# Optimization experiments

Hardware: AMD Instinct MI355X
Metric: run time of the kernel (lower is better)

The kernel has to match this reference:

```python
import jax, jax.numpy as jnp
import numpy as np

B, N, F_IN, F_OUT = 64, 1024, 200, 200
NEG_SLOPE = 0.2  # PyG GATConv default


def setup_inputs() -> dict:
    key = jax.random.key(0)
    k1, k2, k3, k4, k5 = jax.random.split(key, 5)
    return {
        "x": jax.random.normal(k1, (B, 1, N, F_IN), dtype=jnp.float32),
        "W": jax.random.normal(k2, (F_IN, F_OUT), dtype=jnp.float32) * 0.05,
        "att_src": jax.random.normal(k3, (F_OUT,), dtype=jnp.float32) * 0.05,
        "att_dst": jax.random.normal(k4, (F_OUT,), dtype=jnp.float32) * 0.05,
        "bias": jax.random.normal(k5, (F_OUT,), dtype=jnp.float32) * 0.05,
    }


def reference(x, W, att_src, att_dst, bias):
    # x: [B, 1, N, F_IN]; module flattens to (B*N) nodes but the edge_index
    # only spans node ids 0..N-1 (complete graph minus self loops). PyG's
    # GATConv re-adds self loops for ALL B*N nodes, so:
    #   nodes 0..N-1 : dense softmax attention over all N nodes (incl. self)
    #   nodes >= N   : only the self loop -> out = h_i + bias
    b, _, n, f = x.shape
    xf = x.reshape(b * n, f)
    h = xf @ W                                # [B*N, F_OUT] linear transform

    h0 = h[:n]                                # first graph's nodes
    a_s = h0 @ att_src                        # [N] per-source score
    a_d = h0 @ att_dst                        # [N] per-target score
    # score[i, j] = leaky_relu(a_dst[i] + a_src[j]), softmax over sources j
    scores = jax.nn.leaky_relu(a_d[:, None] + a_s[None, :], negative_slope=NEG_SLOPE)
    alpha = jax.nn.softmax(scores, axis=1)    # [N, N]
    out0 = alpha @ h0 + bias                  # [N, F_OUT]

    out_rest = h[n:] + bias                   # self-loop only -> alpha == 1
    out = jnp.concatenate([out0, out_rest], axis=0)
    return out.reshape(b, n, -1)[:, None]     # [B, 1, N, F_OUT]
```

## Files before the change

kernel.cpp:

```cpp
#include <hip/hip_runtime.h>

#define BATCH 64
#define NNODE 1024
#define FDIM  200
#define MROWS (BATCH * NNODE)
#define NEG_SLOPE 0.2f

#define NKT 7
#define NNT 13
#define FRAGW_BYTES (NKT * NNT * 1024)

typedef short s16x8 __attribute__((ext_vector_type(8)));
typedef float f32x4 __attribute__((ext_vector_type(4)));


__device__ __forceinline__ unsigned int f2bf(float f) {
    unsigned int u = __float_as_uint(f);
    return (u + 0x7fffu + ((u >> 16) & 1u)) >> 16;
}
__device__ __forceinline__ unsigned int pack2(float a, float b) {
    return f2bf(a) | (f2bf(b) << 16);
}
__device__ __forceinline__ float lrelu(float s) {
    return (s > 0.f) ? s : NEG_SLOPE * s;
}

__global__ __launch_bounds__(64) void k_prep(const float* __restrict__ W,
                                             const float* __restrict__ att_src,
                                             const float* __restrict__ att_dst,
                                             unsigned short* __restrict__ fragW,
                                             float* __restrict__ wsv,
                                             float* __restrict__ wdv)
{
    const int b    = blockIdx.x;
    const int lane = threadIdx.x;

    if (b < 91) {
        const int kt   = b / NNT;
        const int nt   = b - kt * NNT;
        const int n    = nt * 16 + (lane & 15);
        const int kb   = kt * 32 + (lane >> 4) * 8;
        s16x8 v;
        #pragma unroll
        for (int j = 0; j < 8; ++j) {
            int k = kb + j;
            float f = (k < FDIM && n < FDIM) ? W[k * FDIM + n] : 0.f;
            v[j] = (short)f2bf(f);
        }
        ((s16x8*)(fragW + (size_t)b * 512))[lane] = v;
    } else {
        const int kk = b - 91;
        const float* Wr = W + kk * FDIM;
        float ps = 0.f, pd = 0.f;
        #pragma unroll
        for (int i = 0; i < 4; ++i) {
            int n = lane + i * 64;
            if (n < FDIM) {
                float wv = Wr[n];
                ps = fmaf(wv, att_src[n], ps);
                pd = fmaf(wv, att_dst[n], pd);
            }
        }
        #pragma unroll
        for (int off = 32; off; off >>= 1) {
            ps += __shfl_down(ps, off);
            pd += __shfl_down(pd, off);
        }
        if (lane == 0) { wsv[kk] = ps; wdv[kk] = pd; }
    }
}

__global__ __launch_bounds__(512, 2) void k_gemm(const float* __restrict__ x,
                                                 const unsigned short* __restrict__ fragW,
                                                 const float* __restrict__ bias,
                                                 const float* __restrict__ wsv,
                                                 const float* __restrict__ wdv,
                                                 float* __restrict__ out,
                                                 unsigned short* __restrict__ h0frag,
                                                 float* __restrict__ a_s,
                                                 float* __restrict__ a_d)
{
    __shared__ __align__(16) unsigned short Bf[FRAGW_BYTES / 2];
    __shared__ float scr[8][16 * 17];
    const int tid  = threadIdx.x;
    const int lane = tid & 63;
    const int w    = __builtin_amdgcn_readfirstlane(tid >> 6);
    const int ln   = lane & 15;
    const int quad = lane >> 4;
    const int R0   = blockIdx.x * 128;
    const int row0 = R0 + w * 16;

    {
        const char* gsrc = (const char*)fragW;
        char* ldst = (char*)&Bf[0];
        #pragma unroll
        for (int r = 0; r < 12; ++r) {
            int off = tid * 16 + r * 8192;
            if (off < FRAGW_BYTES)
                __builtin_amdgcn_global_load_lds(
                    (const __attribute__((address_space(1))) void*)(gsrc + off),
                    (__attribute__((address_space(3))) void*)(ldst + off),
                    16, 0, 0);
        }
    }

    const float* xrow = x + (size_t)(row0 + ln) * FDIM;
    float4 ar[NKT][2];
    #pragma unroll
    for (int kt = 0; kt < NKT; ++kt) {
        if (kt < 6) {
            const float4* ap = (const float4*)(xrow + kt * 32 + quad * 8);
            ar[kt][0] = ap[0]; ar[kt][1] = ap[1];
        } else {
            if (quad == 0) {
                const float4* ap = (const float4*)(xrow + kt * 32);
                ar[kt][0] = ap[0]; ar[kt][1] = ap[1];
            } else {
                ar[kt][0] = make_float4(0.f, 0.f, 0.f, 0.f);
                ar[kt][1] = make_float4(0.f, 0.f, 0.f, 0.f);
            }
        }
    }

    f32x4 acc[NNT];
    #pragma unroll
    for (int nt = 0; nt < NNT; ++nt) acc[nt] = (f32x4){0.f, 0.f, 0.f, 0.f};

    __syncthreads();

    #pragma unroll
    for (int kt = 0; kt < NKT; ++kt) {
        float4 f0 = ar[kt][0], f1 = ar[kt][1];
        unsigned int au[4] = {pack2(f0.x, f0.y), pack2(f0.z, f0.w),
                              pack2(f1.x, f1.y), pack2(f1.z, f1.w)};
        s16x8 a = *(s16x8*)au;
        const unsigned short* bbase = &Bf[kt * NNT * 512];
        #pragma unroll
        for (int nt = 0; nt < NNT; ++nt) {
            s16x8 b = *(const s16x8*)(bbase + nt * 512 + lane * 8);
            acc[nt] = __builtin_amdgcn_mfma_f32_16x16x32_bf16(a, b, acc[nt], 0, 0, 0);
        }
    }

    if (R0 >= NNODE) {
        #pragma unroll
        for (int nt = 0; nt < NNT; ++nt) {
            int col = nt * 16 + ln;
            if (nt < 12 || ln < 8) {
                float bv = bias[col];
                #pragma unroll
                for (int r = 0; r < 4; ++r)
                    out[(size_t)(row0 + quad * 4 + r) * FDIM + col] = acc[nt][r] + bv;
            }
        }
    } else {
        {
            float ps = 0.f, pd = 0.f;
            #pragma unroll
            for (int kt = 0; kt < NKT; ++kt) {
                if (kt < 6 || quad == 0) {
                    float4 f0 = ar[kt][0], f1 = ar[kt][1];
                    const float4* sp = (const float4*)(wsv + kt * 32 + quad * 8);
                    const float4* dp = (const float4*)(wdv + kt * 32 + quad * 8);
                    float4 s0 = sp[0], s1 = sp[1], d0 = dp[0], d1 = dp[1];
                    ps += f0.x*s0.x + f0.y*s0.y + f0.z*s0.z + f0.w*s0.w
                        + f1.x*s1.x + f1.y*s1.y + f1.z*s1.z + f1.w*s1.w;
                    pd += f0.x*d0.x + f0.y*d0.y + f0.z*d0.z + f0.w*d0.w
                        + f1.x*d1.x + f1.y*d1.y + f1.z*d1.z + f1.w*d1.w;
                }
            }
            ps += __shfl_down(ps, 32); ps += __shfl_down(ps, 16);
            pd += __shfl_down(pd, 32); pd += __shfl_down(pd, 16);
            if (lane < 16) {
                a_s[row0 + lane] = ps;
                a_d[row0 + lane] = pd;
            }
        }
        float* scrw = &scr[w][0];
        const int kt2 = row0 >> 5;
        const int lo  = (row0 >> 4) & 1;
        for (int nt = 0; nt < NNT; ++nt) {
            #pragma unroll
            for (int r = 0; r < 4; ++r) scrw[(quad * 4 + r) * 17 + ln] = acc[nt][r];
            __syncthreads();
            if (lane < 32) {
                int oct = lane >> 4, nl = lane & 15;
                uint4 dv;
                dv.x = pack2(scrw[(oct * 8 + 0) * 17 + nl], scrw[(oct * 8 + 1) * 17 + nl]);
                dv.y = pack2(scrw[(oct * 8 + 2) * 17 + nl], scrw[(oct * 8 + 3) * 17 + nl]);
                dv.z = pack2(scrw[(oct * 8 + 4) * 17 + nl], scrw[(oct * 8 + 5) * 17 + nl]);
                dv.w = pack2(scrw[(oct * 8 + 6) * 17 + nl], scrw[(oct * 8 + 7) * 17 + nl]);
                *(uint4*)(h0frag + ((size_t)(kt2 * NNT + nt) * 64 + lo * 32 + lane) * 8) = dv;
            }
            __syncthreads();
        }
    }
}

__global__ __launch_bounds__(256) void k_attn(const unsigned short* __restrict__ h0frag,
                                              const float* __restrict__ a_s,
                                              const float* __restrict__ a_d,
                                              const float* __restrict__ bias,
                                              float* __restrict__ out)
{
    __shared__ __align__(16) float as_s[1024];
    __shared__ float mls[16];
    __shared__ float rls[16];
    __shared__ f32x4 red[3][64];
    const int tid  = threadIdx.x;
    const int lane = tid & 63;
    const int w    = __builtin_amdgcn_readfirstlane(tid >> 6);
    const int ln   = lane & 15;
    const int quad = lane >> 4;
    const int it   = blockIdx.x / NNT;
    const int nt   = blockIdx.x - it * NNT;
    const int i0   = it * 16;

    #pragma unroll
    for (int i = 0; i < 4; ++i) as_s[tid + i * 256] = a_s[tid + i * 256];
    __syncthreads();

    float mx = -1e30f;
    #pragma unroll
    for (int i = 0; i < 16; ++i) mx = fmaxf(mx, as_s[lane + i * 64]);
    #pragma unroll
    for (int off = 32; off; off >>= 1) mx = fmaxf(mx, __shfl_down(mx, off));
    mx = __shfl(mx, 0);

    #pragma unroll
    for (int rr = 0; rr < 4; ++rr) {
        const int r  = w * 4 + rr;
        const float adr = a_d[i0 + r];
        const float mi  = lrelu(adr + mx);
        float sum = 0.f;
        #pragma unroll
        for (int i = 0; i < 16; ++i)
            sum += __expf(lrelu(adr + as_s[lane + i * 64]) - mi);
        #pragma unroll
        for (int off = 32; off; off >>= 1) sum += __shfl_down(sum, off);
        if (lane == 0) { mls[r] = mi; rls[r] = 1.0f / sum; }
    }
    __syncthreads();

    const float ad = a_d[i0 + ln];
    const float mi = mls[ln];

    f32x4 accA = (f32x4){0.f, 0.f, 0.f, 0.f};
    f32x4 accB = (f32x4){0.f, 0.f, 0.f, 0.f};

    #pragma unroll
    for (int k8 = 0; k8 < 8; ++k8) {
        const int kt2 = w * 8 + k8;
        const float4* ap = (const float4*)(as_s + kt2 * 32 + quad * 8);
        float4 f0 = ap[0], f1 = ap[1];
        float e[8] = {f0.x, f0.y, f0.z, f0.w, f1.x, f1.y, f1.z, f1.w};
        #pragma unroll
        for (int j = 0; j < 8; ++j)
            e[j] = __expf(lrelu(ad + e[j]) - mi);
        unsigned int au[4] = {pack2(e[0], e[1]), pack2(e[2], e[3]),
                              pack2(e[4], e[5]), pack2(e[6], e[7])};
        s16x8 afrag = *(s16x8*)au;
        s16x8 b = *(const s16x8*)(h0frag + ((size_t)(kt2 * NNT + nt) * 64 + lane) * 8);
        if (k8 & 1) accB = __builtin_amdgcn_mfma_f32_16x16x32_bf16(afrag, b, accB, 0, 0, 0);
        else        accA = __builtin_amdgcn_mfma_f32_16x16x32_bf16(afrag, b, accA, 0, 0, 0);
    }

    f32x4 acc = accA + accB;
    if (w > 0) red[w - 1][lane] = acc;
    __syncthreads();

    if (w == 0) {
        #pragma unroll
        for (int ww = 0; ww < 3; ++ww) acc += red[ww][lane];
        const int col = nt * 16 + ln;
        if (nt < 12 || ln < 8) {
            float bv = bias[col];
            #pragma unroll
            for (int r = 0; r < 4; ++r) {
                float rl = rls[quad * 4 + r];
                out[(size_t)(i0 + quad * 4 + r) * FDIM + col] = acc[r] * rl + bv;
            }
        }
    }
}

extern "C" void kernel_launch(void* const* d_in, const int* in_sizes, int n_in,
                              void* d_out, int out_size, void* d_ws, size_t ws_size,
                              hipStream_t stream)
{
    const float* x       = (const float*)d_in[0];
    const float* W       = (const float*)d_in[1];
    const float* att_src = (const float*)d_in[2];
    const float* att_dst = (const float*)d_in[3];
    const float* bias    = (const float*)d_in[4];
    float* out = (float*)d_out;
    char*  wsb = (char*)d_ws;

    unsigned short* h0frag = (unsigned short*)(wsb + 0);
    float* a_s   = (float*)(wsb + 425984);
    float* a_d   = (float*)(wsb + 430080);
    unsigned short* fragW = (unsigned short*)(wsb + 442368);
    float* wsv   = (float*)(wsb + 535552);
    float* wdv   = (float*)(wsb + 536352);

    k_prep <<<291,          64, 0, stream>>>(W, att_src, att_dst, fragW, wsv, wdv);
    k_gemm <<<MROWS / 128, 512, 0, stream>>>(x, fragW, bias, wsv, wdv, out, h0frag, a_s, a_d);
    k_attn <<<64 * NNT,    256, 0, stream>>>(h0frag, a_s, a_d, bias, out);
}
```

Baseline: 128.5 us.

## Process two row tiles per GEMM block to amortize LDS weight loads

Halves the k_gemm grid so each block computes two 128-row tiles, reusing the bf16 weight fragments already staged in LDS. The second tile's x rows are prefetched into registers before the first tile's MFMA loop to overlap global loads with compute. This removes half the redundant weight-to-LDS traffic and block launch overhead, at the cost of higher register pressure and fewer blocks in flight.

```diff
diff --git a/kernel.cpp b/kernel.cpp
--- a/kernel.cpp
+++ b/kernel.cpp
@@ -9,6 +9,7 @@
 #define NKT 7
 #define NNT 13
 #define FRAGW_BYTES (NKT * NNT * 1024)
+#define NBLK 256
 
 typedef short s16x8 __attribute__((ext_vector_type(8)));
 typedef float f32x4 __attribute__((ext_vector_type(4)));
@@ -87,8 +88,8 @@
     const int w    = __builtin_amdgcn_readfirstlane(tid >> 6);
     const int ln   = lane & 15;
     const int quad = lane >> 4;
-    const int R0   = blockIdx.x * 128;
-    const int row0 = R0 + w * 16;
+    const int row0 = blockIdx.x * 128 + w * 16;
+    const int row1 = (blockIdx.x + NBLK) * 128 + w * 16;
 
     {
         const char* gsrc = (const char*)fragW;
@@ -104,21 +105,20 @@
         }
     }
 
-    const float* xrow = x + (size_t)(row0 + ln) * FDIM;
+    const float* xrow0 = x + (size_t)(row0 + ln) * FDIM;
+    const float* xrow1 = x + (size_t)(row1 + ln) * FDIM;
     float4 ar[NKT][2];
     #pragma unroll
     for (int kt = 0; kt < NKT; ++kt) {
         if (kt < 6) {
-            const float4* ap = (const float4*)(xrow + kt * 32 + quad * 8);
+            const float4* ap = (const float4*)(xrow0 + kt * 32 + quad * 8);
+            ar[kt][0] = ap[0]; ar[kt][1] = ap[1];
+        } else if (quad == 0) {
+            const float4* ap = (const float4*)(xrow0 + kt * 32);
             ar[kt][0] = ap[0]; ar[kt][1] = ap[1];
         } else {
-            if (quad == 0) {
-                const float4* ap = (const float4*)(xrow + kt * 32);
-                ar[kt][0] = ap[0]; ar[kt][1] = ap[1];
-            } else {
-                ar[kt][0] = make_float4(0.f, 0.f, 0.f, 0.f);
-                ar[kt][1] = make_float4(0.f, 0.f, 0.f, 0.f);
-            }
+            ar[kt][0] = make_float4(0.f, 0.f, 0.f, 0.f);
+            ar[kt][1] = make_float4(0.f, 0.f, 0.f, 0.f);
         }
     }
 
@@ -127,6 +127,21 @@
     for (int nt = 0; nt < NNT; ++nt) acc[nt] = (f32x4){0.f, 0.f, 0.f, 0.f};
 
     __syncthreads();
+
+    float4 ar2[NKT][2];
+    #pragma unroll
+    for (int kt = 0; kt < NKT; ++kt) {
+        if (kt < 6) {
+            const float4* ap = (const float4*)(xrow1 + kt * 32 + quad * 8);
+            ar2[kt][0] = ap[0]; ar2[kt][1] = ap[1];
+        } else if (quad == 0) {
+            const float4* ap = (const float4*)(xrow1 + kt * 32);
+            ar2[kt][0] = ap[0]; ar2[kt][1] = ap[1];
+        } else {
+            ar2[kt][0] = make_float4(0.f, 0.f, 0.f, 0.f);
+            ar2[kt][1] = make_float4(0.f, 0.f, 0.f, 0.f);
+        }
+    }
 
     #pragma unroll
     for (int kt = 0; kt < NKT; ++kt) {
@@ -142,7 +157,7 @@
         }
     }
 
-    if (R0 >= NNODE) {
+    if (row0 >= NNODE) {
         #pragma unroll
         for (int nt = 0; nt < NNT; ++nt) {
             int col = nt * 16 + ln;
@@ -193,6 +208,34 @@
                 *(uint4*)(h0frag + ((size_t)(kt2 * NNT + nt) * 64 + lo * 32 + lane) * 8) = dv;
             }
             __syncthreads();
+        }
+    }
+
+    #pragma unroll
+    for (int nt = 0; nt < NNT; ++nt) acc[nt] = (f32x4){0.f, 0.f, 0.f, 0.f};
+
+    #pragma unroll
+    for (int kt = 0; kt < NKT; ++kt) {
+        float4 f0 = ar2[kt][0], f1 = ar2[kt][1];
+        unsigned int au[4] = {pack2(f0.x, f0.y), pack2(f0.z, f0.w),
+                              pack2(f1.x, f1.y), pack2(f1.z, f1.w)};
+        s16x8 a = *(s16x8*)au;
+        const unsigned short* bbase = &Bf[kt * NNT * 512];
+        #pragma unroll
+        for (int nt = 0; nt < NNT; ++nt) {
+            s16x8 b = *(const s16x8*)(bbase + nt * 512 + lane * 8);
+            acc[nt] = __builtin_amdgcn_mfma_f32_16x16x32_bf16(a, b, acc[nt], 0, 0, 0);
+        }
+    }
+
+    #pragma unroll
+    for (int nt = 0; nt < NNT; ++nt) {
+        int col = nt * 16 + ln;
+        if (nt < 12 || ln < 8) {
+            float bv = bias[col];
+            #pragma unroll
+            for (int r = 0; r < 4; ++r)
+                out[(size_t)(row1 + quad * 4 + r) * FDIM + col] = acc[nt][r] + bv;
         }
     }
 }
@@ -303,7 +346,7 @@
     float* wsv   = (float*)(wsb + 535552);
     float* wdv   = (float*)(wsb + 536352);
 
-    k_prep <<<291,          64, 0, stream>>>(W, att_src, att_dst, fragW, wsv, wdv);
-    k_gemm <<<MROWS / 128, 512, 0, stream>>>(x, fragW, bias, wsv, wdv, out, h0frag, a_s, a_d);
-    k_attn <<<64 * NNT,    256, 0, stream>>>(h0frag, a_s, a_d, bias, out);
-}
+    k_prep <<<291,       64, 0, stream>>>(W, att_src, att_dst, fragW, wsv, wdv);
+    k_gemm <<<NBLK,     512, 0, stream>>>(x, fragW, bias, wsv, wdv, out, h0frag, a_s, a_d);
+    k_attn <<<64 * NNT, 256, 0, stream>>>(h0frag, a_s, a_d, bias, out);
+}
```

Result: no change. 128.7 us (+0.1%).
